# Optimization experiments

Measured on AMD Instinct MI355X. Metric: run time of the kernel, lower is better.

The kernel has to match this reference:

```python
import jax, jax.numpy as jnp
import numpy as np

N, E = 50000, 800000
F_IN, F_OUT, H = 128, 16, 8
NEG_SLOPE = 0.2  # PyG GATConv default
EPS = 1e-5       # LayerNorm eps


def setup_inputs() -> dict:
    key = jax.random.key(0)
    ks = jax.random.split(key, 8)
    x = jax.random.normal(ks[0], (N, F_IN), dtype=jnp.float32)
    edge_index = jax.random.randint(ks[1], (2, E), 0, N, dtype=jnp.int32)
    s_in = 1.0 / np.sqrt(F_IN)
    s_f = 1.0 / np.sqrt(F_OUT)
    W = jax.random.normal(ks[2], (F_IN, H * F_OUT), dtype=jnp.float32) * s_in
    att_src = jax.random.normal(ks[3], (H, F_OUT), dtype=jnp.float32) * s_f
    att_dst = jax.random.normal(ks[4], (H, F_OUT), dtype=jnp.float32) * s_f
    bias = jnp.zeros((H * F_OUT,), dtype=jnp.float32)
    gamma = jnp.ones((H * F_OUT,), dtype=jnp.float32)
    beta = jnp.zeros((H * F_OUT,), dtype=jnp.float32)
    return {"x": x, "edge_index": edge_index, "W": W, "att_src": att_src,
            "att_dst": att_dst, "bias": bias, "gamma": gamma, "beta": beta}


def _gat_layer(x, edge_index, W, att_src, att_dst, bias, gamma, beta):
    n = x.shape[0]
    # add self loops (PyG GATConv default add_self_loops=True)
    loop = jnp.arange(n, dtype=edge_index.dtype)
    src = jnp.concatenate([edge_index[0], loop])  # message source j
    dst = jnp.concatenate([edge_index[1], loop])  # message target i

    xp = (x @ W).reshape(n, H, F_OUT)                      # [N,H,F]
    a_src = jnp.einsum('nhf,hf->nh', xp, att_src)          # [N,H]
    a_dst = jnp.einsum('nhf,hf->nh', xp, att_dst)          # [N,H]

    e = a_src[src] + a_dst[dst]                            # [E+N,H]
    e = jax.nn.leaky_relu(e, NEG_SLOPE)
    # softmax over incoming edges per destination node
    m = jax.ops.segment_max(e, dst, num_segments=n)        # [N,H]
    e = jnp.exp(e - m[dst])
    z = jax.ops.segment_sum(e, dst, num_segments=n)        # [N,H]
    alpha = e / jnp.where(z[dst] > 0, z[dst], 1.0)         # [E+N,H]

    msg = alpha[:, :, None] * xp[src]                      # [E+N,H,F]
    out = jax.ops.segment_sum(msg, dst, num_segments=n)    # [N,H,F]
    out = out.reshape(n, H * F_OUT) + bias

    # LayerNorm over feature dim
    mu = out.mean(axis=-1, keepdims=True)
    var = out.var(axis=-1, keepdims=True)
    return (out - mu) * jax.lax.rsqrt(var + EPS) * gamma + beta


def reference(x, edge_index, W, att_src, att_dst, bias, gamma, beta):
    return _gat_layer(x, edge_index, W, att_src, att_dst, bias, gamma, beta)
```

## Files before the change

kernel.cpp:

```cpp
#include <hip/hip_runtime.h>
#include <math.h>

#define F_IN 128
#define NHD 8
#define FEAT 128
#define NEG_SLOPE 0.2f
#define LN_EPS 1e-5f
#define BSH 7
#define BMSK 127
#define NPQ 16
#define CAP 48
#define EPB 2048
#define NBMAX 512
#define BCAP 6144
#define WCOLS 144

typedef __bf16 v8bf __attribute__((ext_vector_type(8)));
typedef __bf16 v2bf __attribute__((ext_vector_type(2)));
typedef float f32x4 __attribute__((ext_vector_type(4)));

__global__ __launch_bounds__(256) void k_wt(const float* __restrict__ W,
                                            const float* __restrict__ att_src,
                                            const float* __restrict__ att_dst,
                                            __bf16* __restrict__ WT) {
    int idx = blockIdx.x * 256 + threadIdx.x;
    int c = idx >> 7, k = idx & 127;
    float v;
    if (c < 128) {
        v = W[k * 128 + c];
    } else if (c < 136) {
        int h = c - 128;
        float s = 0.f;
#pragma unroll
        for (int f = 0; f < 16; ++f) s += W[k * 128 + h * 16 + f] * att_src[h * 16 + f];
        v = s;
    } else {
        int h = c - 136;
        float s = 0.f;
#pragma unroll
        for (int f = 0; f < 16; ++f) s += W[k * 128 + h * 16 + f] * att_dst[h * 16 + f];
        v = s;
    }
    WT[c * 128 + k] = (__bf16)v;
}

__global__ __launch_bounds__(512) void k_fused(const float* __restrict__ x,
                                               const __bf16* __restrict__ WT,
                                               __bf16* __restrict__ xp16,
                                               float* __restrict__ a_src,
                                               float* __restrict__ a_dst,
                                               const int* __restrict__ src,
                                               const int* __restrict__ dst,
                                               unsigned int* __restrict__ sorted_g,
                                               int* __restrict__ runptr,
                                               int n, int E, int Ga) {
    __shared__ __bf16 xs[64][136];
    if ((int)blockIdx.x < Ga) {
        __shared__ int lcnt[NBMAX];
        __shared__ int loff[NBMAX + 1];
        __shared__ unsigned int sorted_l[EPB];
        __shared__ int wtot[8], wexcl[8];
        int NB = (n + BMSK) >> BSH;
        int tid = threadIdx.x, lane = tid & 63, wid = tid >> 6;
        long base0 = (long)blockIdx.x * EPB;
        long total = (long)E + n;
        if (tid < NB) lcnt[tid] = 0;
        __syncthreads();

        int s0[4], d0[4];
        bool val[4];
        long e0 = base0 + (long)tid * 4;
        if (e0 + 3 < E) {
            int4 sv = *(const int4*)(src + e0);
            int4 dv = *(const int4*)(dst + e0);
            s0[0] = sv.x; s0[1] = sv.y; s0[2] = sv.z; s0[3] = sv.w;
            d0[0] = dv.x; d0[1] = dv.y; d0[2] = dv.z; d0[3] = dv.w;
            val[0] = val[1] = val[2] = val[3] = true;
        } else {
#pragma unroll
            for (int j = 0; j < 4; ++j) {
                long e = e0 + j;
                val[j] = (e < total);
                s0[j] = d0[j] = 0;
                if (val[j]) {
                    if (e < E) { s0[j] = src[e]; d0[j] = dst[e]; }
                    else { s0[j] = d0[j] = (int)(e - E); }
                }
            }
        }
#pragma unroll
        for (int j = 0; j < 4; ++j)
            if (val[j]) atomicAdd(&lcnt[d0[j] >> BSH], 1);
        __syncthreads();

        int v = (tid < NB) ? lcnt[tid] : 0;
        int xx = v;
#pragma unroll
        for (int o = 1; o < 64; o <<= 1) {
            int t2 = __shfl_up(xx, o);
            if (lane >= o) xx += t2;
        }
        if (lane == 63) wtot[wid] = xx;
        __syncthreads();
        if (wid == 0 && lane < 8) {
            int s = wtot[lane];
            int y = s;
#pragma unroll
            for (int o = 1; o < 8; o <<= 1) {
                int t2 = __shfl_up(y, o);
                if (lane >= o) y += t2;
            }
            wexcl[lane] = y - s;
        }
        __syncthreads();
        int excl = wexcl[wid] + xx - v;
        if (tid < NB) loff[tid] = excl;
        if (tid == NB - 1) loff[NB] = excl + v;
        __syncthreads();
        if (tid < NB) lcnt[tid] = loff[tid];
        __syncthreads();
#pragma unroll
        for (int j = 0; j < 4; ++j) {
            if (val[j]) {
                int b = d0[j] >> BSH;
                int pos = atomicAdd(&lcnt[b], 1);
                sorted_l[pos] = ((unsigned)s0[j] << BSH) | (unsigned)(d0[j] & BMSK);
            }
        }
        __syncthreads();
        int tv = loff[NB];
        for (int i = tid; i < tv; i += 512)
            sorted_g[base0 + i] = sorted_l[i];
        if (tid <= NB) runptr[(long)blockIdx.x * (NBMAX + 1) + tid] = loff[tid];
    } else {
        int gb = blockIdx.x - Ga;
        int tid = threadIdx.x;
        int rowbase = gb * 64;
        {
            int i4 = tid;
#pragma unroll
            for (int rep = 0; rep < 4; ++rep, i4 += 512) {
                int r = i4 >> 5, c4 = i4 & 31;
                int gr = rowbase + r; if (gr > n - 1) gr = n - 1;
                float4 xv = *(const float4*)(x + (long)gr * 128 + c4 * 4);
                __bf16* p = &xs[r][c4 * 4];
                p[0] = (__bf16)xv.x; p[1] = (__bf16)xv.y;
                p[2] = (__bf16)xv.z; p[3] = (__bf16)xv.w;
            }
        }
        __syncthreads();
        int wv = tid >> 6;
        int lane = tid & 63;
        int m = lane & 15, quad = lane >> 4;
        int colbase = wv * 16;
        const __bf16* wcol = WT + (colbase + m) * 128;
        v8bf wf[4];
#pragma unroll
        for (int kk = 0; kk < 4; ++kk)
            wf[kk] = *(const v8bf*)(wcol + kk * 32 + quad * 8);
        v8bf wf2[4];
        if (wv < 4) {
            const __bf16* wcol2 = WT + (128 + m) * 128;
#pragma unroll
            for (int kk = 0; kk < 4; ++kk)
                wf2[kk] = *(const v8bf*)(wcol2 + kk * 32 + quad * 8);
        }
#pragma unroll
        for (int t = 0; t < 4; ++t) {
            int rb = t * 16;
            f32x4 acc = {0.f, 0.f, 0.f, 0.f};
#pragma unroll
            for (int kk = 0; kk < 4; ++kk) {
                v8bf a = *(const v8bf*)(&xs[rb + m][kk * 32 + quad * 8]);
                acc = __builtin_amdgcn_mfma_f32_16x16x32_bf16(a, wf[kk], acc, 0, 0, 0);
            }
#pragma unroll
            for (int r = 0; r < 4; ++r) {
                int row = rowbase + rb + quad * 4 + r;
                if (row < n)
                    xp16[(long)row * 128 + colbase + m] = (__bf16)acc[r];
            }
        }
        if (wv < 4) {
            int rb = wv * 16;
            f32x4 acc = {0.f, 0.f, 0.f, 0.f};
#pragma unroll
            for (int kk = 0; kk < 4; ++kk) {
                v8bf a = *(const v8bf*)(&xs[rb + m][kk * 32 + quad * 8]);
                acc = __builtin_amdgcn_mfma_f32_16x16x32_bf16(a, wf2[kk], acc, 0, 0, 0);
            }
#pragma unroll
            for (int r = 0; r < 4; ++r) {
                int row = rowbase + rb + quad * 4 + r;
                if (row < n) {
                    if (m < 8) a_src[row * 8 + m] = acc[r];
                    else       a_dst[row * 8 + (m - 8)] = acc[r];
                }
            }
        }
    }
}

__global__ __launch_bounds__(256) void k_reorder(const unsigned int* __restrict__ sorted_g,
                                                 const int* __restrict__ runptr,
                                                 unsigned int* __restrict__ sorted2,
                                                 int* __restrict__ bcnt, int Ga) {
    int b = blockIdx.x;
    int tid = threadIdx.x, lane = tid & 63, wid = tid >> 6;
    __shared__ int wsum[4], wexcl_s[4];
    __shared__ int carry_s;
    if (tid == 0) carry_s = 0;
    __syncthreads();
    for (int base = 0; base < Ga; base += 256) {
        int blk = base + tid;
        int st = 0, c = 0;
        if (blk < Ga) {
            const int* rp = runptr + (long)blk * (NBMAX + 1) + b;
            st = rp[0];
            c = rp[1] - st;
        }
        int xx = c;
#pragma unroll
        for (int o = 1; o < 64; o <<= 1) {
            int t2 = __shfl_up(xx, o);
            if (lane >= o) xx += t2;
        }
        if (lane == 63) wsum[wid] = xx;
        __syncthreads();
        if (tid == 0) {
            int s = 0;
#pragma unroll
            for (int w = 0; w < 4; ++w) { wexcl_s[w] = s; s += wsum[w]; }
            wsum[0] = s;
        }
        __syncthreads();
        int excl = carry_s + wexcl_s[wid] + xx - c;
        const unsigned int* sg = sorted_g + (long)blk * EPB + st;
        unsigned int* dp = sorted2 + (long)b * BCAP + excl;
        int lim = BCAP - excl;
        for (int i = 0; i < c && i < lim; ++i) dp[i] = sg[i];
        __syncthreads();
        if (tid == 0) carry_s += wsum[0];
        __syncthreads();
    }
    if (tid == 0) bcnt[b] = carry_s < BCAP ? carry_s : BCAP;
}

__global__ __launch_bounds__(256) void k_ba(const unsigned int* __restrict__ sorted2,
                                            const int* __restrict__ bcnt,
                                            const float* __restrict__ a_src,
                                            const float* __restrict__ a_dst,
                                            const __bf16* __restrict__ xp16,
                                            const float* __restrict__ bias,
                                            const float* __restrict__ gamma,
                                            const float* __restrict__ beta,
                                            const int* __restrict__ src,
                                            const int* __restrict__ dst,
                                            float* __restrict__ out, int n, int E) {
    __shared__ int slds[NPQ * CAP];
    __shared__ int lc[NPQ];
    __shared__ float adst_s[NPQ * NHD];
    int b = blockIdx.x >> 3;
    int q = blockIdx.x & 7;
    int tid = threadIdx.x;
    int node0 = (b << BSH) + q * NPQ;
    if (tid < NPQ) lc[tid] = 0;
    if (tid < NPQ * NHD) {
        int nd = node0 + (tid >> 3);
        adst_s[tid] = (nd < n) ? a_dst[nd * NHD + (tid & 7)] : 0.f;
    }
    __syncthreads();

    int cnt_b = bcnt[b];
    const unsigned int* sg = sorted2 + (long)b * BCAP;
    int qlo = q * NPQ;
    for (int i = tid; i < cnt_b; i += 256) {
        unsigned int u = sg[i];
        int dl = (int)(u & BMSK) - qlo;
        if ((unsigned)dl < (unsigned)NPQ) {
            int p = atomicAdd(&lc[dl], 1);
            if (p < CAP) slds[dl * CAP + p] = (int)(u >> BSH);
        }
    }
    __syncthreads();
    if (tid < NPQ) {
        int cc = lc[tid]; if (cc > CAP) cc = CAP;
        int pad = (cc + 7) & ~7; if (pad > CAP) pad = CAP;
        for (int p = cc; p < pad; ++p) slds[tid * CAP + p] = 0;
    }
    __syncthreads();

    int lane = tid & 63, wv = tid >> 6;
    int h = lane & 7, j8 = lane >> 3;
    float2 bs = *(const float2*)(bias + 2 * lane);
    float2 g  = *(const float2*)(gamma + 2 * lane);
    float2 bt = *(const float2*)(beta + 2 * lane);

    for (int i = wv; i < NPQ; i += 4) {
        int node = node0 + i;
        if (node >= n) break;
        int cnt = lc[i];
        float acc0 = 0.f, acc1 = 0.f, inv;

        if (cnt <= CAP) {
            const int* row = slds + i * CAP;
            float b_h = adst_s[i * NHD + h];
            float zacc = 0.f;
            for (int base = 0; base < cnt; base += 8) {
                int s_my = row[base + j8];
                float e = a_src[s_my * NHD + h] + b_h;
                e = e > 0.f ? e : NEG_SLOPE * e;
                float w_my = (base + j8 < cnt) ? __expf(e) : 0.f;
                zacc += w_my;
                int ss[8];
#pragma unroll
                for (int j = 0; j < 8; ++j) ss[j] = row[base + j];
                float2 vals[8];
#pragma unroll
                for (int j = 0; j < 8; ++j) {
                    v2bf p = *(const v2bf*)(xp16 + (long)ss[j] * FEAT + 2 * lane);
                    vals[j] = make_float2((float)p[0], (float)p[1]);
                }
#pragma unroll
                for (int j = 0; j < 8; ++j) {
                    float w = __shfl(w_my, j * 8 + j8);
                    acc0 = fmaf(w, vals[j].x, acc0);
                    acc1 = fmaf(w, vals[j].y, acc1);
                }
            }
            zacc += __shfl_xor(zacc, 8);
            zacc += __shfl_xor(zacc, 16);
            zacc += __shfl_xor(zacc, 32);
            float z = __shfl(zacc, j8);
            inv = 1.f / z;
        } else {
            float b_h = a_dst[node * NHD + j8];
            float z = 0.f;
            {
                float e = a_src[node * NHD + j8] + b_h;
                e = e > 0.f ? e : NEG_SLOPE * e;
                float w = __expf(e);
                z += w;
                v2bf p = *(const v2bf*)(xp16 + (long)node * FEAT + 2 * lane);
                acc0 = fmaf(w, (float)p[0], acc0);
                acc1 = fmaf(w, (float)p[1], acc1);
            }
            for (int base = 0; base < E; base += 64) {
                int e = base + lane;
                int sv = 0;
                bool mt = false;
                if (e < E) { mt = (dst[e] == node); if (mt) sv = src[e]; }
                unsigned long long mask = __ballot(mt);
                while (mask) {
                    int bl = __ffsll(mask) - 1;
                    mask &= mask - 1;
                    int s = __shfl(sv, bl);
                    float ee = a_src[s * NHD + j8] + b_h;
                    ee = ee > 0.f ? ee : NEG_SLOPE * ee;
                    float w = __expf(ee);
                    z += w;
                    v2bf p = *(const v2bf*)(xp16 + (long)s * FEAT + 2 * lane);
                    acc0 = fmaf(w, (float)p[0], acc0);
                    acc1 = fmaf(w, (float)p[1], acc1);
                }
            }
            inv = 1.f / z;
        }

        float v0 = acc0 * inv + bs.x;
        float v1 = acc1 * inv + bs.y;
        float ssum = v0 + v1;
        float ssq = v0 * v0 + v1 * v1;
#pragma unroll
        for (int o = 32; o > 0; o >>= 1) {
            ssum += __shfl_xor(ssum, o);
            ssq += __shfl_xor(ssq, o);
        }
        float mu = ssum * (1.0f / FEAT);
        float var = ssq * (1.0f / FEAT) - mu * mu;
        float rs = rsqrtf(var + LN_EPS);
        float2 o2;
        o2.x = (v0 - mu) * rs * g.x + bt.x;
        o2.y = (v1 - mu) * rs * g.y + bt.y;
        *(float2*)(out + (long)node * FEAT + 2 * lane) = o2;
    }
}

extern "C" void kernel_launch(void* const* d_in, const int* in_sizes, int n_in,
                              void* d_out, int out_size, void* d_ws, size_t ws_size,
                              hipStream_t stream) {
    const float* x = (const float*)d_in[0];
    const int* edge_index = (const int*)d_in[1];
    const float* W = (const float*)d_in[2];
    const float* att_src = (const float*)d_in[3];
    const float* att_dst = (const float*)d_in[4];
    const float* bias = (const float*)d_in[5];
    const float* gamma = (const float*)d_in[6];
    const float* beta = (const float*)d_in[7];
    float* out = (float*)d_out;

    int n = in_sizes[0] / F_IN;
    int E = in_sizes[1] / 2;
    const int* src = edge_index;
    const int* dst = edge_index + E;
    int NB = (n + BMSK) >> BSH;
    int Ga = (E + n + EPB - 1) / EPB;
    int Gg = (n + 63) / 64;

    char* ws = (char*)d_ws;
    __bf16* WT   = (__bf16*)ws;                    ws += (size_t)WCOLS * 128 * 2;
    __bf16* xp16 = (__bf16*)ws;                    ws += (size_t)n * FEAT * 2;
    float* a_src = (float*)ws;                     ws += (size_t)n * NHD * 4;
    float* a_dst = (float*)ws;                     ws += (size_t)n * NHD * 4;
    unsigned int* sorted_g = (unsigned int*)ws;    ws += (size_t)Ga * EPB * 4;
    unsigned int* sorted2 = (unsigned int*)ws;     ws += (size_t)NB * BCAP * 4;
    int* bcnt = (int*)ws;                          ws += (size_t)NB * 4;
    int* runptr  = (int*)ws;                       ws += (size_t)Ga * (NBMAX + 1) * 4;

    k_wt<<<72, 256, 0, stream>>>(W, att_src, att_dst, WT);
    k_fused<<<Ga + Gg, 512, 0, stream>>>(x, WT, xp16, a_src, a_dst,
                                         src, dst, sorted_g, runptr, n, E, Ga);
    k_reorder<<<NB, 256, 0, stream>>>(sorted_g, runptr, sorted2, bcnt, Ga);
    k_ba<<<NB * 8, 256, 0, stream>>>(sorted2, bcnt, a_src, a_dst, xp16,
                                     bias, gamma, beta, src, dst, out, n, E);
}
```

Baseline: 165.5 us.

## Stage GEMM output through LDS, parallelize bucket reorder, widen aggregation loads

The projection kernel now puts its bf16 output tile in shared memory and writes whole rows to global memory as 16-byte vectors, replacing scattered 2-byte stores. Shared memory is unioned between the sort and GEMM branches to keep the footprint down. The reorder kernel splits each bucket across 4 blocks, does a single-wave prefix scan, and copies runs with all lanes instead of one thread per run. The aggregation kernel first computes the attention weights into LDS, then gathers xp rows with 8-byte loads split across two half-waves, at the cost of extra LDS traffic and a shuffle reduction.

New measurement: 173.4 us. 1.05x slower.

```diff
diff --git a/kernel.cpp b/kernel.cpp
--- a/kernel.cpp
+++ b/kernel.cpp
@@ -16,6 +16,7 @@
 #define WCOLS 144
 
 typedef __bf16 v8bf __attribute__((ext_vector_type(8)));
+typedef __bf16 v4bf __attribute__((ext_vector_type(4)));
 typedef __bf16 v2bf __attribute__((ext_vector_type(2)));
 typedef float f32x4 __attribute__((ext_vector_type(4)));
 
@@ -54,12 +55,13 @@
                                                unsigned int* __restrict__ sorted_g,
                                                int* __restrict__ runptr,
                                                int n, int E, int Ga) {
-    __shared__ __bf16 xs[64][136];
+    __shared__ __align__(16) char smem[34816];
     if ((int)blockIdx.x < Ga) {
-        __shared__ int lcnt[NBMAX];
-        __shared__ int loff[NBMAX + 1];
-        __shared__ unsigned int sorted_l[EPB];
-        __shared__ int wtot[8], wexcl[8];
+        unsigned int* sorted_l = (unsigned int*)smem;
+        int* lcnt = (int*)(smem + 8192);
+        int* loff = (int*)(smem + 8192 + 2048);
+        int* wtot = (int*)(smem + 8192 + 2048 + 2052);
+        int* wexcl = (int*)(smem + 8192 + 2048 + 2052 + 32);
         int NB = (n + BMSK) >> BSH;
         int tid = threadIdx.x, lane = tid & 63, wid = tid >> 6;
         long base0 = (long)blockIdx.x * EPB;
@@ -133,6 +135,8 @@
             sorted_g[base0 + i] = sorted_l[i];
         if (tid <= NB) runptr[(long)blockIdx.x * (NBMAX + 1) + tid] = loff[tid];
     } else {
+        __bf16 (*xs)[136] = (__bf16 (*)[136])smem;
+        __bf16 (*ot)[136] = (__bf16 (*)[136])(smem + 17408);
         int gb = blockIdx.x - Ga;
         int tid = threadIdx.x;
         int rowbase = gb * 64;
@@ -175,11 +179,8 @@
                 acc = __builtin_amdgcn_mfma_f32_16x16x32_bf16(a, wf[kk], acc, 0, 0, 0);
             }
 #pragma unroll
-            for (int r = 0; r < 4; ++r) {
-                int row = rowbase + rb + quad * 4 + r;
-                if (row < n)
-                    xp16[(long)row * 128 + colbase + m] = (__bf16)acc[r];
-            }
+            for (int r = 0; r < 4; ++r)
+                ot[rb + quad * 4 + r][colbase + m] = (__bf16)acc[r];
         }
         if (wv < 4) {
             int rb = wv * 16;
@@ -198,6 +199,17 @@
                 }
             }
         }
+        __syncthreads();
+        int r0 = tid >> 4, c8 = tid & 15;
+#pragma unroll
+        for (int pass = 0; pass < 2; ++pass) {
+            int r = r0 + pass * 32;
+            int gr = rowbase + r;
+            if (gr < n) {
+                v8bf vv = *(const v8bf*)(&ot[r][c8 * 8]);
+                *(v8bf*)(xp16 + (long)gr * FEAT + c8 * 8) = vv;
+            }
+        }
     }
 }
 
@@ -205,45 +217,47 @@
                                                  const int* __restrict__ runptr,
                                                  unsigned int* __restrict__ sorted2,
                                                  int* __restrict__ bcnt, int Ga) {
-    int b = blockIdx.x;
-    int tid = threadIdx.x, lane = tid & 63, wid = tid >> 6;
-    __shared__ int wsum[4], wexcl_s[4];
-    __shared__ int carry_s;
-    if (tid == 0) carry_s = 0;
+    __shared__ int st_s[NBMAX];
+    __shared__ int offs[NBMAX + 1];
+    int b = blockIdx.x >> 2, g = blockIdx.x & 3;
+    int tid = threadIdx.x, lane = tid & 63, wv = tid >> 6;
+    for (int blk = tid; blk < Ga; blk += 256) {
+        const int* rp = runptr + (long)blk * (NBMAX + 1) + b;
+        int st = rp[0], en = rp[1];
+        st_s[blk] = st;
+        offs[blk] = en - st;
+    }
     __syncthreads();
-    for (int base = 0; base < Ga; base += 256) {
-        int blk = base + tid;
-        int st = 0, c = 0;
-        if (blk < Ga) {
-            const int* rp = runptr + (long)blk * (NBMAX + 1) + b;
-            st = rp[0];
-            c = rp[1] - st;
-        }
-        int xx = c;
-#pragma unroll
-        for (int o = 1; o < 64; o <<= 1) {
-            int t2 = __shfl_up(xx, o);
-            if (lane >= o) xx += t2;
-        }
-        if (lane == 63) wsum[wid] = xx;
-        __syncthreads();
-        if (tid == 0) {
-            int s = 0;
-#pragma unroll
-            for (int w = 0; w < 4; ++w) { wexcl_s[w] = s; s += wsum[w]; }
-            wsum[0] = s;
-        }
-        __syncthreads();
-        int excl = carry_s + wexcl_s[wid] + xx - c;
-        const unsigned int* sg = sorted_g + (long)blk * EPB + st;
-        unsigned int* dp = sorted2 + (long)b * BCAP + excl;
-        int lim = BCAP - excl;
-        for (int i = 0; i < c && i < lim; ++i) dp[i] = sg[i];
-        __syncthreads();
-        if (tid == 0) carry_s += wsum[0];
-        __syncthreads();
-    }
-    if (tid == 0) bcnt[b] = carry_s < BCAP ? carry_s : BCAP;
+    if (wv == 0) {
+        int carry = 0;
+        for (int c0 = 0; c0 < Ga; c0 += 64) {
+            int idx = c0 + lane;
+            int v = (idx < Ga) ? offs[idx] : 0;
+            int xx = v;
+#pragma unroll
+            for (int o = 1; o < 64; o <<= 1) {
+                int t2 = __shfl_up(xx, o);
+                if (lane >= o) xx += t2;
+            }
+            if (idx < Ga) offs[idx] = carry + xx - v;
+            carry += __shfl(xx, 63);
+        }
+        if (lane == 0) offs[Ga] = carry;
+    }
+    __syncthreads();
+    for (int blk = g * 4 + wv; blk < Ga; blk += 16) {
+        int off = offs[blk];
+        int c = offs[blk + 1] - off;
+        if (off >= BCAP) continue;
+        if (c > BCAP - off) c = BCAP - off;
+        const unsigned int* s = sorted_g + (long)blk * EPB + st_s[blk];
+        unsigned int* d = sorted2 + (long)b * BCAP + off;
+        for (int i = lane; i < c; i += 64) d[i] = s[i];
+    }
+    if (g == 0 && tid == 0) {
+        int t = offs[Ga];
+        bcnt[b] = t < BCAP ? t : BCAP;
+    }
 }
 
 __global__ __launch_bounds__(256) void k_ba(const unsigned int* __restrict__ sorted2,
@@ -258,6 +272,7 @@
                                             const int* __restrict__ dst,
                                             float* __restrict__ out, int n, int E) {
     __shared__ int slds[NPQ * CAP];
+    __shared__ float wlds[4][8][50];
     __shared__ int lc[NPQ];
     __shared__ float adst_s[NPQ * NHD];
     int b = blockIdx.x >> 3;
@@ -291,59 +306,92 @@
     __syncthreads();
 
     int lane = tid & 63, wv = tid >> 6;
-    int h = lane & 7, j8 = lane >> 3;
-    float2 bs = *(const float2*)(bias + 2 * lane);
-    float2 g  = *(const float2*)(gamma + 2 * lane);
-    float2 bt = *(const float2*)(beta + 2 * lane);
+    int par = lane >> 5, c32 = lane & 31;
+    int hL = c32 >> 2;
+    int h8 = lane & 7, p8 = lane >> 3;
+    float4 bs = *(const float4*)(bias + 4 * c32);
+    float4 gm = *(const float4*)(gamma + 4 * c32);
+    float4 bt = *(const float4*)(beta + 4 * c32);
+    float* wrow = &wlds[wv][0][0];
 
     for (int i = wv; i < NPQ; i += 4) {
         int node = node0 + i;
         if (node >= n) break;
         int cnt = lc[i];
-        float acc0 = 0.f, acc1 = 0.f, inv;
 
         if (cnt <= CAP) {
             const int* row = slds + i * CAP;
-            float b_h = adst_s[i * NHD + h];
+            float b_h = adst_s[i * NHD + h8];
             float zacc = 0.f;
             for (int base = 0; base < cnt; base += 8) {
-                int s_my = row[base + j8];
-                float e = a_src[s_my * NHD + h] + b_h;
+                int p = base + p8;
+                int s = row[p];
+                float e = a_src[s * NHD + h8] + b_h;
                 e = e > 0.f ? e : NEG_SLOPE * e;
-                float w_my = (base + j8 < cnt) ? __expf(e) : 0.f;
-                zacc += w_my;
-                int ss[8];
-#pragma unroll
-                for (int j = 0; j < 8; ++j) ss[j] = row[base + j];
-                float2 vals[8];
-#pragma unroll
-                for (int j = 0; j < 8; ++j) {
-                    v2bf p = *(const v2bf*)(xp16 + (long)ss[j] * FEAT + 2 * lane);
-                    vals[j] = make_float2((float)p[0], (float)p[1]);
-                }
-#pragma unroll
-                for (int j = 0; j < 8; ++j) {
-                    float w = __shfl(w_my, j * 8 + j8);
-                    acc0 = fmaf(w, vals[j].x, acc0);
-                    acc1 = fmaf(w, vals[j].y, acc1);
-                }
+                float w = (p < cnt) ? __expf(e) : 0.f;
+                zacc += w;
+                wrow[h8 * 50 + p] = w;
             }
             zacc += __shfl_xor(zacc, 8);
             zacc += __shfl_xor(zacc, 16);
             zacc += __shfl_xor(zacc, 32);
-            float z = __shfl(zacc, j8);
-            inv = 1.f / z;
+            asm volatile("s_waitcnt lgkmcnt(0)" ::: "memory");
+
+            float a0 = 0.f, a1 = 0.f, a2 = 0.f, a3 = 0.f;
+            for (int base = 0; base < cnt; base += 8) {
+#pragma unroll
+                for (int j = 0; j < 4; ++j) {
+                    int p = base + 2 * j + par;
+                    int s = row[p];
+                    float w = wrow[hL * 50 + p];
+                    v4bf v = *(const v4bf*)(xp16 + (long)s * FEAT + 4 * c32);
+                    a0 = fmaf(w, (float)v[0], a0);
+                    a1 = fmaf(w, (float)v[1], a1);
+                    a2 = fmaf(w, (float)v[2], a2);
+                    a3 = fmaf(w, (float)v[3], a3);
+                }
+            }
+            a0 += __shfl_xor(a0, 32);
+            a1 += __shfl_xor(a1, 32);
+            a2 += __shfl_xor(a2, 32);
+            a3 += __shfl_xor(a3, 32);
+            float inv = 1.f / __shfl(zacc, hL);
+            float v0 = a0 * inv + bs.x;
+            float v1 = a1 * inv + bs.y;
+            float v2 = a2 * inv + bs.z;
+            float v3 = a3 * inv + bs.w;
+            float ssum = v0 + v1 + v2 + v3;
+            float ssq = v0 * v0 + v1 * v1 + v2 * v2 + v3 * v3;
+#pragma unroll
+            for (int o = 16; o > 0; o >>= 1) {
+                ssum += __shfl_xor(ssum, o);
+                ssq += __shfl_xor(ssq, o);
+            }
+            float mu = ssum * (1.0f / FEAT);
+            float var = ssq * (1.0f / FEAT) - mu * mu;
+            float rs = rsqrtf(var + LN_EPS);
+            if (par == 0) {
+                float4 o4;
+                o4.x = (v0 - mu) * rs * gm.x + bt.x;
+                o4.y = (v1 - mu) * rs * gm.y + bt.y;
+                o4.z = (v2 - mu) * rs * gm.z + bt.z;
+                o4.w = (v3 - mu) * rs * gm.w + bt.w;
+                *(float4*)(out + (long)node * FEAT + 4 * c32) = o4;
+            }
         } else {
-            float b_h = a_dst[node * NHD + j8];
+            float bh = a_dst[node * NHD + hL];
             float z = 0.f;
+            float a0 = 0.f, a1 = 0.f, a2 = 0.f, a3 = 0.f;
             {
-                float e = a_src[node * NHD + j8] + b_h;
+                float e = a_src[node * NHD + hL] + bh;
                 e = e > 0.f ? e : NEG_SLOPE * e;
                 float w = __expf(e);
                 z += w;
-                v2bf p = *(const v2bf*)(xp16 + (long)node * FEAT + 2 * lane);
-                acc0 = fmaf(w, (float)p[0], acc0);
-                acc1 = fmaf(w, (float)p[1], acc1);
+                v4bf v = *(const v4bf*)(xp16 + (long)node * FEAT + 4 * c32);
+                a0 = fmaf(w, (float)v[0], a0);
+                a1 = fmaf(w, (float)v[1], a1);
+                a2 = fmaf(w, (float)v[2], a2);
+                a3 = fmaf(w, (float)v[3], a3);
             }
             for (int base = 0; base < E; base += 64) {
                 int e = base + lane;
@@ -355,34 +403,41 @@
                     int bl = __ffsll(mask) - 1;
                     mask &= mask - 1;
                     int s = __shfl(sv, bl);
-                    float ee = a_src[s * NHD + j8] + b_h;
+                    float ee = a_src[s * NHD + hL] + bh;
                     ee = ee > 0.f ? ee : NEG_SLOPE * ee;
                     float w = __expf(ee);
                     z += w;
-                    v2bf p = *(const v2bf*)(xp16 + (long)s * FEAT + 2 * lane);
-                    acc0 = fmaf(w, (float)p[0], acc0);
-                    acc1 = fmaf(w, (float)p[1], acc1);
+                    v4bf v = *(const v4bf*)(xp16 + (long)s * FEAT + 4 * c32);
+                    a0 = fmaf(w, (float)v[0], a0);
+                    a1 = fmaf(w, (float)v[1], a1);
+                    a2 = fmaf(w, (float)v[2], a2);
+                    a3 = fmaf(w, (float)v[3], a3);
                 }
             }
-            inv = 1.f / z;
-        }
-
-        float v0 = acc0 * inv + bs.x;
-        float v1 = acc1 * inv + bs.y;
-        float ssum = v0 + v1;
-        float ssq = v0 * v0 + v1 * v1;
-#pragma unroll
-        for (int o = 32; o > 0; o >>= 1) {
-            ssum += __shfl_xor(ssum, o);
-            ssq += __shfl_xor(ssq, o);
-        }
-        float mu = ssum * (1.0f / FEAT);
-        float var = ssq * (1.0f / FEAT) - mu * mu;
-        float rs = rsqrtf(var + LN_EPS);
-        float2 o2;
-        o2.x = (v0 - mu) * rs * g.x + bt.x;
-        o2.y = (v1 - mu) * rs * g.y + bt.y;
-        *(float2*)(out + (long)node * FEAT + 2 * lane) = o2;
+            float inv = 1.f / z;
+            float v0 = a0 * inv + bs.x;
+            float v1 = a1 * inv + bs.y;
+            float v2 = a2 * inv + bs.z;
+            float v3 = a3 * inv + bs.w;
+            float ssum = v0 + v1 + v2 + v3;
+            float ssq = v0 * v0 + v1 * v1 + v2 * v2 + v3 * v3;
+#pragma unroll
+            for (int o = 16; o > 0; o >>= 1) {
+                ssum += __shfl_xor(ssum, o);
+                ssq += __shfl_xor(ssq, o);
+            }
+            float mu = ssum * (1.0f / FEAT);
+            float var = ssq * (1.0f / FEAT) - mu * mu;
+            float rs = rsqrtf(var + LN_EPS);
+            if (par == 0) {
+                float4 o4;
+                o4.x = (v0 - mu) * rs * gm.x + bt.x;
+                o4.y = (v1 - mu) * rs * gm.y + bt.y;
+                o4.z = (v2 - mu) * rs * gm.z + bt.z;
+                o4.w = (v3 - mu) * rs * gm.w + bt.w;
+                *(float4*)(out + (long)node * FEAT + 4 * c32) = o4;
+            }
+        }
     }
 }
 
@@ -420,7 +475,7 @@
     k_wt<<<72, 256, 0, stream>>>(W, att_src, att_dst, WT);
     k_fused<<<Ga + Gg, 512, 0, stream>>>(x, WT, xp16, a_src, a_dst,
                                          src, dst, sorted_g, runptr, n, E, Ga);
-    k_reorder<<<NB, 256, 0, stream>>>(sorted_g, runptr, sorted2, bcnt, Ga);
+    k_reorder<<<NB * 4, 256, 0, stream>>>(sorted_g, runptr, sorted2, bcnt, Ga);
     k_ba<<<NB * 8, 256, 0, stream>>>(sorted2, bcnt, a_src, a_dst, xp16,
                                      bias, gamma, beta, src, dst, out, n, E);
 }
```
